# Kernel tuning notes

Measured on AMD Instinct MI355X. Metric: run time of the kernel, lower is better.

Reference implementation:

```python
import jax, jax.numpy as jnp
import numpy as np

NUM_HEADS = 4
HIDDEN = 128
LN_EPS = 1e-6
NEG_INF = -1e9


def setup_inputs() -> dict:
    key = jax.random.key(0)
    ks = jax.random.split(key, 8)
    B, S, H, NH = 64, 512, HIDDEN, NUM_HEADS
    enc = jax.random.normal(ks[0], (B, S, H), dtype=jnp.float32)
    mask = jax.random.randint(ks[1], (B, 1, S, S), 0, 2, dtype=jnp.int32)
    scale = 1.0 / np.sqrt(H)
    # torch Linear(H, H*NH, bias=False): weight is (H*NH, H); store transposed (H, H*NH)
    Wq = jax.random.normal(ks[2], (H, H * NH), dtype=jnp.float32) * scale
    Wk = jax.random.normal(ks[3], (H, H * NH), dtype=jnp.float32) * scale
    Wv = jax.random.normal(ks[4], (H, H * NH), dtype=jnp.float32) * scale
    Wo = jax.random.normal(ks[5], (H * NH, H), dtype=jnp.float32) * (1.0 / np.sqrt(H * NH))
    gamma = jnp.ones((H,), dtype=jnp.float32)
    beta = jnp.zeros((H,), dtype=jnp.float32)
    return {"enc": enc, "mask": mask, "Wq": Wq, "Wk": Wk, "Wv": Wv, "Wo": Wo, "gamma": gamma, "beta": beta}


def reference(enc, mask, Wq, Wk, Wv, Wo, gamma, beta):
    B, S, H = enc.shape
    NH = NUM_HEADS
    # projections -> (B, NH, S, H): each head has head_dim == hidden_units
    Q = (enc @ Wq).reshape(B, S, NH, H).transpose(0, 2, 1, 3)
    K = (enc @ Wk).reshape(B, S, NH, H).transpose(0, 2, 1, 3)
    V = (enc @ Wv).reshape(B, S, NH, H).transpose(0, 2, 1, 3)
    # scaled dot-product attention with mask (non-flash: full score matrix)
    scores = jnp.einsum('bhqd,bhkd->bhqk', Q, K) / jnp.sqrt(jnp.float32(H))
    scores = jnp.where(mask == 0, jnp.float32(NEG_INF), scores)
    attn = jax.nn.softmax(scores, axis=-1)  # dropout = identity in eval mode
    ctx = jnp.einsum('bhqk,bhkd->bhqd', attn, V)  # (B, NH, S, H)
    ctx = ctx.transpose(0, 2, 1, 3).reshape(B, S, NH * H)
    out = ctx @ Wo + enc  # dropout identity, residual add
    # LayerNorm over last dim
    mu = jnp.mean(out, axis=-1, keepdims=True)
    var = jnp.var(out, axis=-1, keepdims=True)
    return gamma * (out - mu) / jnp.sqrt(var + LN_EPS) + beta
```

## Files before the change

kernel.cpp:

```cpp
#include <hip/hip_runtime.h>
#include <stdint.h>

#define BATCH 64
#define SLEN 512
#define HID 128
#define NHEAD 4
#define DPROJ 512
#define MTOT (BATCH * SLEN)
#define SCALE 0.08838834764831845f

using short8 = __attribute__((ext_vector_type(8))) short;
using f32x4  = __attribute__((ext_vector_type(4))) float;
using u32x4  = __attribute__((ext_vector_type(4))) unsigned int;
using u32x2  = __attribute__((ext_vector_type(2))) unsigned int;
using us4    = __attribute__((ext_vector_type(4))) unsigned short;

__device__ __forceinline__ unsigned short f2bf(float f) {
  unsigned int u = __float_as_uint(f);
  u += 0x7fffu + ((u >> 16) & 1u);
  return (unsigned short)(u >> 16);
}

__global__ __launch_bounds__(256) void prep_kernel(
    const float* __restrict__ Wq,
    const float* __restrict__ Wk,
    const float* __restrict__ Wv,
    const float* __restrict__ Wo,
    const float* __restrict__ enc,
    unsigned short* __restrict__ WT,
    unsigned short* __restrict__ WoT,
    unsigned short* __restrict__ encb)
{
  if (blockIdx.x < 1024) {
    int idx = blockIdx.x * 256 + threadIdx.x;
    int z = idx >> 16;
    int i = idx & 65535;
    if (z < 3) {
      const float* W = (z == 0) ? Wq : (z == 1) ? Wk : Wv;
      float scale = (z == 0) ? SCALE : 1.0f;
      int k = i >> 9;
      int n = i & 511;
      WT[(size_t)z * 65536 + (size_t)n * 128 + k] = f2bf(W[i] * scale);
    } else {
      int k = i >> 7;
      int n = i & 127;
      WoT[(size_t)n * 512 + k] = f2bf(Wo[i]);
    }
  } else {
    size_t tid = (size_t)(blockIdx.x - 1024) * 256 + threadIdx.x;
    const float* s = enc + tid * 8;
    f32x4 a0 = *(const f32x4*)(s);
    f32x4 a1 = *(const f32x4*)(s + 4);
    short8 v;
    #pragma unroll
    for (int j = 0; j < 4; ++j) v[j] = (short)f2bf(a0[j]);
    #pragma unroll
    for (int j = 0; j < 4; ++j) v[4 + j] = (short)f2bf(a1[j]);
    *(short8*)(encb + tid * 8) = v;
  }
}

__global__ __launch_bounds__(256) void maskpack_kernel(
    const int* __restrict__ mask,
    unsigned int* __restrict__ mbits)
{
  size_t idx = (size_t)blockIdx.x * 256 + threadIdx.x;
  int m = mask[idx];
  unsigned long long bal = __ballot(m != 0);
  if ((threadIdx.x & 63) == 0)
    *(unsigned long long*)(mbits + (idx >> 5)) = bal;
}

__global__ __launch_bounds__(256) void qkv_kernel(
    const unsigned short* __restrict__ encb,
    const unsigned short* __restrict__ WT,
    unsigned short* __restrict__ Qh,
    unsigned short* __restrict__ Kh,
    unsigned short* __restrict__ Vt)
{
  const int nt = blockIdx.x;
  const int mt = blockIdx.y;
  const int t = threadIdx.x;
  const int lane = t & 63;
  const int w = t >> 6;
  const int quad = lane >> 4;
  const int l16 = lane & 15;

  __shared__ __align__(16) unsigned short Ald[128 * 136];
  __shared__ __align__(16) unsigned short Bld[128 * 136];

  const int m0 = mt * 128, n0 = nt * 128;
  const int wm = (w >> 1) * 64, wn = (w & 1) * 64;

  #pragma unroll
  for (int i = 0; i < 8; ++i) {
    int idx = i * 256 + t;
    int row = idx >> 4;
    int col = (idx & 15) << 3;
    *(u32x4*)(Ald + row * 136 + col) =
        *(const u32x4*)(encb + (size_t)(m0 + row) * HID + col);
  }

  for (int z = 0; z < 3; ++z) {
    __syncthreads();
    const unsigned short* Wz = WT + (size_t)z * DPROJ * HID;
    #pragma unroll
    for (int i = 0; i < 8; ++i) {
      int idx = i * 256 + t;
      int row = idx >> 4;
      int col = (idx & 15) << 3;
      *(u32x4*)(Bld + row * 136 + col) =
          *(const u32x4*)(Wz + (size_t)(n0 + row) * HID + col);
    }
    __syncthreads();

    f32x4 acc[4][4];
    #pragma unroll
    for (int mi = 0; mi < 4; ++mi)
      #pragma unroll
      for (int ni = 0; ni < 4; ++ni)
        acc[mi][ni] = f32x4{0.f, 0.f, 0.f, 0.f};

    #pragma unroll
    for (int kk = 0; kk < 4; ++kk) {
      short8 a[4], bb[4];
      #pragma unroll
      for (int mi = 0; mi < 4; ++mi)
        a[mi] = *(const short8*)(Ald + (wm + mi * 16 + l16) * 136 + kk * 32 + quad * 8);
      #pragma unroll
      for (int ni = 0; ni < 4; ++ni)
        bb[ni] = *(const short8*)(Bld + (wn + ni * 16 + l16) * 136 + kk * 32 + quad * 8);
      if (z < 2) {
        #pragma unroll
        for (int mi = 0; mi < 4; ++mi)
          #pragma unroll
          for (int ni = 0; ni < 4; ++ni)
            acc[mi][ni] = __builtin_amdgcn_mfma_f32_16x16x32_bf16(bb[ni], a[mi], acc[mi][ni], 0, 0, 0);
      } else {
        #pragma unroll
        for (int mi = 0; mi < 4; ++mi)
          #pragma unroll
          for (int ni = 0; ni < 4; ++ni)
            acc[mi][ni] = __builtin_amdgcn_mfma_f32_16x16x32_bf16(a[mi], bb[ni], acc[mi][ni], 0, 0, 0);
      }
    }

    if (z < 2) {
      unsigned short* outz = ((z == 0) ? Qh : Kh) + (size_t)nt * MTOT * HID;
      #pragma unroll
      for (int mi = 0; mi < 4; ++mi)
        #pragma unroll
        for (int ni = 0; ni < 4; ++ni) {
          int m = m0 + wm + mi * 16 + l16;
          int dbase = wn + ni * 16 + quad * 4;
          us4 pk;
          #pragma unroll
          for (int r = 0; r < 4; ++r) pk[r] = f2bf(acc[mi][ni][r]);
          *(us4*)(outz + (size_t)m * HID + dbase) = pk;
        }
    } else {
      #pragma unroll
      for (int mi = 0; mi < 4; ++mi)
        #pragma unroll
        for (int ni = 0; ni < 4; ++ni) {
          int row0 = m0 + wm + mi * 16 + quad * 4;
          int b = row0 >> 9, s = row0 & 511;
          int d = wn + ni * 16 + l16;
          us4 pk;
          #pragma unroll
          for (int r = 0; r < 4; ++r) pk[r] = f2bf(acc[mi][ni][r]);
          *(us4*)(Vt + ((size_t)(nt * BATCH + b) * HID + d) * SLEN + s) = pk;
        }
    }
  }
}

__global__ __launch_bounds__(512, 4) void attn_kernel(
    const unsigned short* __restrict__ Qh,
    const unsigned short* __restrict__ Kh,
    const unsigned short* __restrict__ Vt,
    const unsigned int* __restrict__ mbits,
    unsigned short* __restrict__ ctx)
{
  const int lin = blockIdx.x;
  const int work = (lin & 7) * 128 + (lin >> 3);
  const int qt = work & 3;
  const int h  = (work >> 2) & 3;
  const int b  = work >> 4;

  const int t = threadIdx.x;
  const int lane = t & 63;
  const int w = t >> 6;
  const int quad = lane >> 4;
  const int l16 = lane & 15;

  __shared__ __align__(16) unsigned short Kld[64 * 136];
  __shared__ __align__(16) unsigned short Vtld[128 * 72];
  __shared__ __align__(16) unsigned short Pld[128 * 72];

  const int q0 = qt * 128;
  const size_t rowbase = (size_t)b * SLEN;
  const unsigned short* kbase0 = Kh + ((size_t)h * MTOT + rowbase) * HID;
  const unsigned short* vbase  = Vt + (size_t)(h * BATCH + b) * HID * SLEN;
  const unsigned int* mrow = mbits + (size_t)b * SLEN * 16;

  const int k_key = t >> 4,           k_col = (t & 15) << 3;
  const int v_d   = t >> 3,           v_cc  = (t & 7) << 3;

  short8 qa[4];
  {
    const unsigned short* qbase =
        Qh + ((size_t)h * MTOT + rowbase + q0 + w * 16 + l16) * HID + quad * 8;
    #pragma unroll
    for (int kk = 0; kk < 4; ++kk)
      qa[kk] = *(const short8*)(qbase + kk * 32);
  }

  short8 ones;
  #pragma unroll
  for (int j = 0; j < 8; ++j) ones[j] = (short)0x3F80;

  f32x4 oc[8], oc9;
  #pragma unroll
  for (int nd = 0; nd < 8; ++nd) oc[nd] = f32x4{0.f, 0.f, 0.f, 0.f};
  oc9 = f32x4{0.f, 0.f, 0.f, 0.f};

  u32x4 kreg[2], vreg[2];
  #pragma unroll
  for (int i = 0; i < 2; ++i) {
    kreg[i] = *(const u32x4*)(kbase0 + (size_t)(k_key + i * 32) * HID + k_col);
    vreg[i] = *(const u32x4*)(vbase + (size_t)(v_d + i * 64) * SLEN + v_cc);
  }

  for (int c0 = 0; c0 < SLEN; c0 += 64) {
    if (c0) __syncthreads();
    #pragma unroll
    for (int i = 0; i < 2; ++i) {
      *(u32x4*)(Kld + (k_key + i * 32) * 136 + k_col) = kreg[i];
      *(u32x4*)(Vtld + (v_d + i * 64) * 72 + v_cc) = vreg[i];
    }
    __syncthreads();
    if (c0 + 64 < SLEN) {
      #pragma unroll
      for (int i = 0; i < 2; ++i) {
        kreg[i] = *(const u32x4*)(kbase0 + (size_t)(c0 + 64 + k_key + i * 32) * HID + k_col);
        vreg[i] = *(const u32x4*)(vbase + (size_t)(v_d + i * 64) * SLEN + c0 + 64 + v_cc);
      }
    }

    u32x2 mw[4];
    #pragma unroll
    for (int r = 0; r < 4; ++r) {
      int qrow = q0 + w * 16 + quad * 4 + r;
      mw[r] = *(const u32x2*)(mrow + (size_t)qrow * 16 + (c0 >> 5));
    }

    f32x4 sc[4];
    #pragma unroll
    for (int ni = 0; ni < 4; ++ni) sc[ni] = f32x4{0.f, 0.f, 0.f, 0.f};
    #pragma unroll
    for (int kk = 0; kk < 4; ++kk) {
      #pragma unroll
      for (int ni = 0; ni < 4; ++ni) {
        short8 bb = *(const short8*)(Kld + (ni * 16 + l16) * 136 + kk * 32 + quad * 8);
        sc[ni] = __builtin_amdgcn_mfma_f32_16x16x32_bf16(qa[kk], bb, sc[ni], 0, 0, 0);
      }
    }

    #pragma unroll
    for (int ni = 0; ni < 4; ++ni) {
      int bit = (ni & 1) * 16 + l16;
      #pragma unroll
      for (int r = 0; r < 4; ++r) {
        unsigned wsel = (ni < 2) ? mw[r][0] : mw[r][1];
        float e = __expf(sc[ni][r]);
        float p = ((wsel >> bit) & 1u) ? e : 0.f;
        Pld[(w * 16 + quad * 4 + r) * 72 + ni * 16 + l16] = f2bf(p);
      }
    }
    __threadfence_block();

    #pragma unroll
    for (int kb = 0; kb < 2; ++kb) {
      short8 a = *(const short8*)(Pld + (w * 16 + l16) * 72 + kb * 32 + quad * 8);
      #pragma unroll
      for (int nd = 0; nd < 8; ++nd) {
        short8 bv = *(const short8*)(Vtld + (nd * 16 + l16) * 72 + kb * 32 + quad * 8);
        oc[nd] = __builtin_amdgcn_mfma_f32_16x16x32_bf16(a, bv, oc[nd], 0, 0, 0);
      }
      oc9 = __builtin_amdgcn_mfma_f32_16x16x32_bf16(a, ones, oc9, 0, 0, 0);
    }
  }

  #pragma unroll
  for (int nd = 0; nd < 8; ++nd)
    #pragma unroll
    for (int r = 0; r < 4; ++r) {
      float val = oc[nd][r] / oc9[r];
      int row = q0 + w * 16 + quad * 4 + r;
      int col = h * HID + nd * 16 + l16;
      ctx[(rowbase + row) * DPROJ + col] = f2bf(val);
    }
}

__global__ __launch_bounds__(256, 4) void oproj_ln_kernel(
    const unsigned short* __restrict__ ctx,
    const unsigned short* __restrict__ WoT,
    const float* __restrict__ enc,
    const float* __restrict__ gamma,
    const float* __restrict__ beta,
    float* __restrict__ out)
{
  const int m0 = blockIdx.x * 64;
  const int t = threadIdx.x;
  const int lane = t & 63;
  const int w = t >> 6;
  const int quad = lane >> 4;
  const int l16 = lane & 15;

  __shared__ __align__(16) unsigned short Actx[64 * 72];
  __shared__ __align__(16) unsigned short Bw[128 * 72];

  f32x4 acc[8];
  #pragma unroll
  for (int ni = 0; ni < 8; ++ni) acc[ni] = f32x4{0.f, 0.f, 0.f, 0.f};

  for (int kc = 0; kc < DPROJ; kc += 64) {
    __syncthreads();
    #pragma unroll
    for (int i = 0; i < 2; ++i) {
      int idx = i * 256 + t;
      int row = idx >> 3;
      int col = (idx & 7) << 3;
      *(u32x4*)(Actx + row * 72 + col) =
          *(const u32x4*)(ctx + (size_t)(m0 + row) * DPROJ + kc + col);
    }
    #pragma unroll
    for (int i = 0; i < 4; ++i) {
      int idx = i * 256 + t;
      int row = idx >> 3;
      int col = (idx & 7) << 3;
      *(u32x4*)(Bw + row * 72 + col) =
          *(const u32x4*)(WoT + (size_t)row * DPROJ + kc + col);
    }
    __syncthreads();
    #pragma unroll
    for (int kk = 0; kk < 2; ++kk) {
      short8 a = *(const short8*)(Actx + (w * 16 + l16) * 72 + kk * 32 + quad * 8);
      #pragma unroll
      for (int ni = 0; ni < 8; ++ni) {
        short8 bb = *(const short8*)(Bw + (ni * 16 + l16) * 72 + kk * 32 + quad * 8);
        acc[ni] = __builtin_amdgcn_mfma_f32_16x16x32_bf16(a, bb, acc[ni], 0, 0, 0);
      }
    }
  }

  float g[8], be[8];
  #pragma unroll
  for (int ni = 0; ni < 8; ++ni) {
    g[ni] = gamma[ni * 16 + l16];
    be[ni] = beta[ni * 16 + l16];
  }

  float val[8][4];
  #pragma unroll
  for (int r = 0; r < 4; ++r) {
    int m = m0 + w * 16 + quad * 4 + r;
    const float* erow = enc + (size_t)m * HID;
    float s = 0.f, s2 = 0.f;
    #pragma unroll
    for (int ni = 0; ni < 8; ++ni) {
      float v = acc[ni][r] + erow[ni * 16 + l16];
      val[ni][r] = v;
      s += v;
      s2 += v * v;
    }
    #pragma unroll
    for (int off = 1; off < 16; off <<= 1) {
      s  += __shfl_xor(s, off, 64);
      s2 += __shfl_xor(s2, off, 64);
    }
    float mean = s * (1.f / 128.f);
    float var = s2 * (1.f / 128.f) - mean * mean;
    float rstd = rsqrtf(var + 1e-6f);
    float* orow = out + (size_t)m * HID;
    #pragma unroll
    for (int ni = 0; ni < 8; ++ni)
      orow[ni * 16 + l16] = g[ni] * (val[ni][r] - mean) * rstd + be[ni];
  }
}

extern "C" void kernel_launch(void* const* d_in, const int* in_sizes, int n_in,
                              void* d_out, int out_size, void* d_ws, size_t ws_size,
                              hipStream_t stream) {
  const float* enc   = (const float*)d_in[0];
  const int*   mask  = (const int*)d_in[1];
  const float* Wq    = (const float*)d_in[2];
  const float* Wk    = (const float*)d_in[3];
  const float* Wv    = (const float*)d_in[4];
  const float* Wo    = (const float*)d_in[5];
  const float* gamma = (const float*)d_in[6];
  const float* beta  = (const float*)d_in[7];
  float* out = (float*)d_out;

  unsigned short* WT  = (unsigned short*)d_ws;
  unsigned short* WoT = WT + (size_t)3 * DPROJ * HID;
  unsigned short* Qh  = WoT + (size_t)HID * DPROJ;
  unsigned short* Kh  = Qh + (size_t)NHEAD * MTOT * HID;
  unsigned short* Vt  = Kh + (size_t)NHEAD * MTOT * HID;
  unsigned short* ctx = Vt + (size_t)NHEAD * MTOT * HID;
  unsigned short* encb = ctx + (size_t)MTOT * DPROJ;
  unsigned int* mbits = (unsigned int*)(encb + (size_t)MTOT * HID * 2);

  prep_kernel<<<3072, 256, 0, stream>>>(Wq, Wk, Wv, Wo, enc, WT, WoT, encb);
  maskpack_kernel<<<65536, 256, 0, stream>>>(mask, mbits);
  qkv_kernel<<<dim3(4, 256), 256, 0, stream>>>(encb, WT, Qh, Kh, Vt);
  attn_kernel<<<1024, 512, 0, stream>>>(Qh, Kh, Vt, mbits, ctx);
  oproj_ln_kernel<<<MTOT / 64, 256, 0, stream>>>(ctx, WoT, enc, gamma, beta, out);
}
```

Before: 256.0 us.

## Split QKV over grid z, swizzle P tile, drop LDS staging in oproj, widen maskpack

```diff
diff --git a/kernel.cpp b/kernel.cpp
--- a/kernel.cpp
+++ b/kernel.cpp
@@ -64,14 +64,19 @@
     const int* __restrict__ mask,
     unsigned int* __restrict__ mbits)
 {
-  size_t idx = (size_t)blockIdx.x * 256 + threadIdx.x;
-  int m = mask[idx];
-  unsigned long long bal = __ballot(m != 0);
-  if ((threadIdx.x & 63) == 0)
-    *(unsigned long long*)(mbits + (idx >> 5)) = bal;
-}
-
-__global__ __launch_bounds__(256) void qkv_kernel(
+  const int l = threadIdx.x & 63;
+  size_t wavebase = (size_t)blockIdx.x * 1024 + (threadIdx.x >> 6) * 256;
+  unsigned long long b0 = __ballot(mask[wavebase + 0 * 64 + l] != 0);
+  unsigned long long b1 = __ballot(mask[wavebase + 1 * 64 + l] != 0);
+  unsigned long long b2 = __ballot(mask[wavebase + 2 * 64 + l] != 0);
+  unsigned long long b3 = __ballot(mask[wavebase + 3 * 64 + l] != 0);
+  if (l < 4) {
+    unsigned long long v = (l & 2) ? ((l & 1) ? b3 : b2) : ((l & 1) ? b1 : b0);
+    *(unsigned long long*)(mbits + (wavebase >> 5) + l * 2) = v;
+  }
+}
+
+__global__ __launch_bounds__(256, 4) void qkv_kernel(
     const unsigned short* __restrict__ encb,
     const unsigned short* __restrict__ WT,
     unsigned short* __restrict__ Qh,
@@ -80,102 +85,90 @@
 {
   const int nt = blockIdx.x;
   const int mt = blockIdx.y;
+  const int z  = blockIdx.z;
   const int t = threadIdx.x;
   const int lane = t & 63;
   const int w = t >> 6;
   const int quad = lane >> 4;
   const int l16 = lane & 15;
 
-  __shared__ __align__(16) unsigned short Ald[128 * 136];
   __shared__ __align__(16) unsigned short Bld[128 * 136];
 
   const int m0 = mt * 128, n0 = nt * 128;
   const int wm = (w >> 1) * 64, wn = (w & 1) * 64;
+  const unsigned short* Wz = WT + (size_t)z * DPROJ * HID;
 
   #pragma unroll
   for (int i = 0; i < 8; ++i) {
     int idx = i * 256 + t;
     int row = idx >> 4;
     int col = (idx & 15) << 3;
-    *(u32x4*)(Ald + row * 136 + col) =
-        *(const u32x4*)(encb + (size_t)(m0 + row) * HID + col);
-  }
-
-  for (int z = 0; z < 3; ++z) {
-    __syncthreads();
-    const unsigned short* Wz = WT + (size_t)z * DPROJ * HID;
-    #pragma unroll
-    for (int i = 0; i < 8; ++i) {
-      int idx = i * 256 + t;
-      int row = idx >> 4;
-      int col = (idx & 15) << 3;
-      *(u32x4*)(Bld + row * 136 + col) =
-          *(const u32x4*)(Wz + (size_t)(n0 + row) * HID + col);
-    }
-    __syncthreads();
-
-    f32x4 acc[4][4];
+    *(u32x4*)(Bld + row * 136 + col) =
+        *(const u32x4*)(Wz + (size_t)(n0 + row) * HID + col);
+  }
+  __syncthreads();
+
+  f32x4 acc[4][4];
+  #pragma unroll
+  for (int mi = 0; mi < 4; ++mi)
+    #pragma unroll
+    for (int ni = 0; ni < 4; ++ni)
+      acc[mi][ni] = f32x4{0.f, 0.f, 0.f, 0.f};
+
+  #pragma unroll
+  for (int kk = 0; kk < 4; ++kk) {
+    short8 a[4], bb[4];
     #pragma unroll
     for (int mi = 0; mi < 4; ++mi)
-      #pragma unroll
-      for (int ni = 0; ni < 4; ++ni)
-        acc[mi][ni] = f32x4{0.f, 0.f, 0.f, 0.f};
-
-    #pragma unroll
-    for (int kk = 0; kk < 4; ++kk) {
-      short8 a[4], bb[4];
-      #pragma unroll
-      for (int mi = 0; mi < 4; ++mi)
-        a[mi] = *(const short8*)(Ald + (wm + mi * 16 + l16) * 136 + kk * 32 + quad * 8);
-      #pragma unroll
-      for (int ni = 0; ni < 4; ++ni)
-        bb[ni] = *(const short8*)(Bld + (wn + ni * 16 + l16) * 136 + kk * 32 + quad * 8);
-      if (z < 2) {
-        #pragma unroll
-        for (int mi = 0; mi < 4; ++mi)
-          #pragma unroll
-          for (int ni = 0; ni < 4; ++ni)
-            acc[mi][ni] = __builtin_amdgcn_mfma_f32_16x16x32_bf16(bb[ni], a[mi], acc[mi][ni], 0, 0, 0);
-      } else {
-        #pragma unroll
-        for (int mi = 0; mi < 4; ++mi)
-          #pragma unroll
-          for (int ni = 0; ni < 4; ++ni)
-            acc[mi][ni] = __builtin_amdgcn_mfma_f32_16x16x32_bf16(a[mi], bb[ni], acc[mi][ni], 0, 0, 0);
-      }
-    }
-
+      a[mi] = *(const short8*)(encb + (size_t)(m0 + wm + mi * 16 + l16) * HID + kk * 32 + quad * 8);
+    #pragma unroll
+    for (int ni = 0; ni < 4; ++ni)
+      bb[ni] = *(const short8*)(Bld + (wn + ni * 16 + l16) * 136 + kk * 32 + quad * 8);
     if (z < 2) {
-      unsigned short* outz = ((z == 0) ? Qh : Kh) + (size_t)nt * MTOT * HID;
       #pragma unroll
       for (int mi = 0; mi < 4; ++mi)
         #pragma unroll
-        for (int ni = 0; ni < 4; ++ni) {
-          int m = m0 + wm + mi * 16 + l16;
-          int dbase = wn + ni * 16 + quad * 4;
-          us4 pk;
-          #pragma unroll
-          for (int r = 0; r < 4; ++r) pk[r] = f2bf(acc[mi][ni][r]);
-          *(us4*)(outz + (size_t)m * HID + dbase) = pk;
-        }
+        for (int ni = 0; ni < 4; ++ni)
+          acc[mi][ni] = __builtin_amdgcn_mfma_f32_16x16x32_bf16(bb[ni], a[mi], acc[mi][ni], 0, 0, 0);
     } else {
       #pragma unroll
       for (int mi = 0; mi < 4; ++mi)
         #pragma unroll
-        for (int ni = 0; ni < 4; ++ni) {
-          int row0 = m0 + wm + mi * 16 + quad * 4;
-          int b = row0 >> 9, s = row0 & 511;
-          int d = wn + ni * 16 + l16;
-          us4 pk;
-          #pragma unroll
-          for (int r = 0; r < 4; ++r) pk[r] = f2bf(acc[mi][ni][r]);
-          *(us4*)(Vt + ((size_t)(nt * BATCH + b) * HID + d) * SLEN + s) = pk;
-        }
-    }
-  }
-}
-
-__global__ __launch_bounds__(512, 4) void attn_kernel(
+        for (int ni = 0; ni < 4; ++ni)
+          acc[mi][ni] = __builtin_amdgcn_mfma_f32_16x16x32_bf16(a[mi], bb[ni], acc[mi][ni], 0, 0, 0);
+    }
+  }
+
+  if (z < 2) {
+    unsigned short* outz = ((z == 0) ? Qh : Kh) + (size_t)nt * MTOT * HID;
+    #pragma unroll
+    for (int mi = 0; mi < 4; ++mi)
+      #pragma unroll
+      for (int ni = 0; ni < 4; ++ni) {
+        int m = m0 + wm + mi * 16 + l16;
+        int dbase = wn + ni * 16 + quad * 4;
+        us4 pk;
+        #pragma unroll
+        for (int r = 0; r < 4; ++r) pk[r] = f2bf(acc[mi][ni][r]);
+        *(us4*)(outz + (size_t)m * HID + dbase) = pk;
+      }
+  } else {
+    #pragma unroll
+    for (int mi = 0; mi < 4; ++mi)
+      #pragma unroll
+      for (int ni = 0; ni < 4; ++ni) {
+        int row0 = m0 + wm + mi * 16 + quad * 4;
+        int b = row0 >> 9, s = row0 & 511;
+        int d = wn + ni * 16 + l16;
+        us4 pk;
+        #pragma unroll
+        for (int r = 0; r < 4; ++r) pk[r] = f2bf(acc[mi][ni][r]);
+        *(us4*)(Vt + ((size_t)(nt * BATCH + b) * HID + d) * SLEN + s) = pk;
+      }
+  }
+}
+
+__global__ __launch_bounds__(512, 6) void attn_kernel(
     const unsigned short* __restrict__ Qh,
     const unsigned short* __restrict__ Kh,
     const unsigned short* __restrict__ Vt,
@@ -196,7 +189,7 @@
 
   __shared__ __align__(16) unsigned short Kld[64 * 136];
   __shared__ __align__(16) unsigned short Vtld[128 * 72];
-  __shared__ __align__(16) unsigned short Pld[128 * 72];
+  __shared__ __align__(16) unsigned short Pld[128 * 64];
 
   const int q0 = qt * 128;
   const size_t rowbase = (size_t)b * SLEN;
@@ -204,8 +197,8 @@
   const unsigned short* vbase  = Vt + (size_t)(h * BATCH + b) * HID * SLEN;
   const unsigned int* mrow = mbits + (size_t)b * SLEN * 16;
 
-  const int k_key = t >> 4,           k_col = (t & 15) << 3;
-  const int v_d   = t >> 3,           v_cc  = (t & 7) << 3;
+  const int k_key = t >> 4, k_col = (t & 15) << 3;
+  const int v_d   = t >> 3, v_cc  = (t & 7) << 3;
 
   short8 qa[4];
   {
@@ -275,35 +268,40 @@
         unsigned wsel = (ni < 2) ? mw[r][0] : mw[r][1];
         float e = __expf(sc[ni][r]);
         float p = ((wsel >> bit) & 1u) ? e : 0.f;
-        Pld[(w * 16 + quad * 4 + r) * 72 + ni * 16 + l16] = f2bf(p);
+        int rowp = w * 16 + quad * 4 + r;
+        int cg = (ni * 2 + (l16 >> 3)) ^ (rowp & 7);
+        Pld[rowp * 64 + cg * 8 + (l16 & 7)] = f2bf(p);
       }
     }
     __threadfence_block();
 
     #pragma unroll
     for (int kb = 0; kb < 2; ++kb) {
-      short8 a = *(const short8*)(Pld + (w * 16 + l16) * 72 + kb * 32 + quad * 8);
+      int rowr = w * 16 + l16;
+      int cg = (kb * 4 + quad) ^ (l16 & 7);
+      short8 a = *(const short8*)(Pld + rowr * 64 + cg * 8);
       #pragma unroll
       for (int nd = 0; nd < 8; ++nd) {
         short8 bv = *(const short8*)(Vtld + (nd * 16 + l16) * 72 + kb * 32 + quad * 8);
-        oc[nd] = __builtin_amdgcn_mfma_f32_16x16x32_bf16(a, bv, oc[nd], 0, 0, 0);
-      }
-      oc9 = __builtin_amdgcn_mfma_f32_16x16x32_bf16(a, ones, oc9, 0, 0, 0);
-    }
-  }
-
-  #pragma unroll
-  for (int nd = 0; nd < 8; ++nd)
-    #pragma unroll
-    for (int r = 0; r < 4; ++r) {
-      float val = oc[nd][r] / oc9[r];
-      int row = q0 + w * 16 + quad * 4 + r;
-      int col = h * HID + nd * 16 + l16;
-      ctx[(rowbase + row) * DPROJ + col] = f2bf(val);
-    }
-}
-
-__global__ __launch_bounds__(256, 4) void oproj_ln_kernel(
+        oc[nd] = __builtin_amdgcn_mfma_f32_16x16x32_bf16(bv, a, oc[nd], 0, 0, 0);
+      }
+      oc9 = __builtin_amdgcn_mfma_f32_16x16x32_bf16(ones, a, oc9, 0, 0, 0);
+    }
+  }
+
+  float rcp = 1.0f / oc9[0];
+  int qrow = q0 + w * 16 + l16;
+  unsigned short* crow = ctx + (rowbase + qrow) * DPROJ + h * HID;
+  #pragma unroll
+  for (int nd = 0; nd < 8; ++nd) {
+    us4 pk;
+    #pragma unroll
+    for (int r = 0; r < 4; ++r) pk[r] = f2bf(oc[nd][r] * rcp);
+    *(us4*)(crow + nd * 16 + quad * 4) = pk;
+  }
+}
+
+__global__ __launch_bounds__(256, 2) void oproj_ln_kernel(
     const unsigned short* __restrict__ ctx,
     const unsigned short* __restrict__ WoT,
     const float* __restrict__ enc,
@@ -318,40 +316,19 @@
   const int quad = lane >> 4;
   const int l16 = lane & 15;
 
-  __shared__ __align__(16) unsigned short Actx[64 * 72];
-  __shared__ __align__(16) unsigned short Bw[128 * 72];
+  const unsigned short* arow = ctx + (size_t)(m0 + w * 16 + l16) * DPROJ;
 
   f32x4 acc[8];
   #pragma unroll
   for (int ni = 0; ni < 8; ++ni) acc[ni] = f32x4{0.f, 0.f, 0.f, 0.f};
 
-  for (int kc = 0; kc < DPROJ; kc += 64) {
-    __syncthreads();
-    #pragma unroll
-    for (int i = 0; i < 2; ++i) {
-      int idx = i * 256 + t;
-      int row = idx >> 3;
-      int col = (idx & 7) << 3;
-      *(u32x4*)(Actx + row * 72 + col) =
-          *(const u32x4*)(ctx + (size_t)(m0 + row) * DPROJ + kc + col);
-    }
-    #pragma unroll
-    for (int i = 0; i < 4; ++i) {
-      int idx = i * 256 + t;
-      int row = idx >> 3;
-      int col = (idx & 7) << 3;
-      *(u32x4*)(Bw + row * 72 + col) =
-          *(const u32x4*)(WoT + (size_t)row * DPROJ + kc + col);
-    }
-    __syncthreads();
-    #pragma unroll
-    for (int kk = 0; kk < 2; ++kk) {
-      short8 a = *(const short8*)(Actx + (w * 16 + l16) * 72 + kk * 32 + quad * 8);
-      #pragma unroll
-      for (int ni = 0; ni < 8; ++ni) {
-        short8 bb = *(const short8*)(Bw + (ni * 16 + l16) * 72 + kk * 32 + quad * 8);
-        acc[ni] = __builtin_amdgcn_mfma_f32_16x16x32_bf16(a, bb, acc[ni], 0, 0, 0);
-      }
+  #pragma unroll
+  for (int kc = 0; kc < 16; ++kc) {
+    short8 a = *(const short8*)(arow + kc * 32 + quad * 8);
+    #pragma unroll
+    for (int ni = 0; ni < 8; ++ni) {
+      short8 bb = *(const short8*)(WoT + (size_t)(ni * 16 + l16) * DPROJ + kc * 32 + quad * 8);
+      acc[ni] = __builtin_amdgcn_mfma_f32_16x16x32_bf16(a, bb, acc[ni], 0, 0, 0);
     }
   }
 
@@ -413,8 +390,8 @@
   unsigned int* mbits = (unsigned int*)(encb + (size_t)MTOT * HID * 2);
 
   prep_kernel<<<3072, 256, 0, stream>>>(Wq, Wk, Wv, Wo, enc, WT, WoT, encb);
-  maskpack_kernel<<<65536, 256, 0, stream>>>(mask, mbits);
-  qkv_kernel<<<dim3(4, 256), 256, 0, stream>>>(encb, WT, Qh, Kh, Vt);
+  maskpack_kernel<<<16384, 256, 0, stream>>>(mask, mbits);
+  qkv_kernel<<<dim3(4, 256, 3), 256, 0, stream>>>(encb, WT, Qh, Kh, Vt);
   attn_kernel<<<1024, 512, 0, stream>>>(Qh, Kh, Vt, mbits, ctx);
   oproj_ln_kernel<<<MTOT / 64, 256, 0, stream>>>(ctx, WoT, enc, gamma, beta, out);
 }
```

Result: slower. 486.9 us (+90.2%).
